# Kernel tuning notes

Hardware: AMD Instinct MI355X
Metric: run time of the kernel (lower is better)

The kernel has to match this reference:

```python
import jax, jax.numpy as jnp
import numpy as np

N_NODES = 100000
N_EDGES = 1600000
IN, HID, OUT = 128, 256, 64
EPS = 0.0  # init_eps=0, learn_eps=False


def setup_inputs() -> dict:
    key = jax.random.key(0)
    k1, k2, k3, k4, k5 = jax.random.split(key, 5)
    x = jax.random.normal(k1, (N_NODES, IN), dtype=jnp.float32)
    edge_src = jax.random.randint(k2, (N_EDGES,), 0, N_NODES, dtype=jnp.int64)
    edge_dst = jax.random.randint(k3, (N_EDGES,), 0, N_NODES, dtype=jnp.int64)
    W1 = jax.random.normal(k4, (IN, HID), dtype=jnp.float32) * (1.0 / np.sqrt(IN))
    W2 = jax.random.normal(k5, (HID, OUT), dtype=jnp.float32) * (1.0 / np.sqrt(HID))
    return {"x": x, "edge_src": edge_src, "edge_dst": edge_dst, "W1": W1, "W2": W2}


def _gin_conv(h, edge_src, edge_dst, W, n_nodes):
    # sum aggregation of messages h[src] into dst, then (1+eps)*h + agg, then linear (no bias)
    agg = jax.ops.segment_sum(h[edge_src], edge_dst, num_segments=n_nodes)
    return ((1.0 + EPS) * h + agg) @ W


def reference(x, edge_src, edge_dst, W1, W2):
    n = x.shape[0]
    h = _gin_conv(x, edge_src, edge_dst, W1, n)   # [N, HID]
    h = _gin_conv(h, edge_src, edge_dst, W2, n)   # [N, OUT]
    return h
```

## Files before the change

kernel.cpp:

```cpp
#include <hip/hip_runtime.h>
#include <hip/hip_bf16.h>

#define IN_F  128
#define HID_F 256
#define OUT_F 64
#define BUCKET_SHIFT 9
#define BUCKET_SZ 512
#define EPB 8192
#define CAP 10240

typedef __attribute__((ext_vector_type(8))) short bf16x8;
typedef __attribute__((ext_vector_type(4))) float f32x4;

__device__ __forceinline__ float bf2f(unsigned short u) {
    union { unsigned int i; float f; } v; v.i = ((unsigned int)u) << 16; return v.f;
}
__device__ __forceinline__ float bf2f_lo(unsigned int p) {
    union { unsigned int i; float f; } v; v.i = p << 16; return v.f;
}
__device__ __forceinline__ float bf2f_hi(unsigned int p) {
    union { unsigned int i; float f; } v; v.i = p & 0xffff0000u; return v.f;
}
__device__ __forceinline__ unsigned short f2bf(float f) {
    __hip_bfloat16 b = __float2bfloat16(f);
    return *reinterpret_cast<unsigned short*>(&b);
}

__global__ __launch_bounds__(256) void k_front(
    const float* __restrict__ x, unsigned short* __restrict__ xb, long long total8,
    const float* __restrict__ W1, const float* __restrict__ W2,
    unsigned short* __restrict__ w12s, int xBlocks)
{
    int bid = blockIdx.x;
    int t = threadIdx.x;
    if (bid < xBlocks) {
        long long i = (long long)bid * 256 + t;
        if (i >= total8) return;
        const float4* p = reinterpret_cast<const float4*>(x) + i * 2;
        float4 a = p[0], b = p[1];
        ushort4 o0, o1;
        o0.x = f2bf(a.x); o0.y = f2bf(a.y); o0.z = f2bf(a.z); o0.w = f2bf(a.w);
        o1.x = f2bf(b.x); o1.y = f2bf(b.y); o1.z = f2bf(b.z); o1.w = f2bf(b.w);
        reinterpret_cast<ushort4*>(xb)[i * 2]     = o0;
        reinterpret_cast<ushort4*>(xb)[i * 2 + 1] = o1;
    } else {
        int idx = (bid - xBlocks) * 256 + t;
        int c = idx >> 9, L = (idx >> 3) & 63, j = idx & 7;
        int nt = c >> 2, ks = c & 3;
        int k = ks * 32 + (L >> 4) * 8 + j;
        int n = nt * 16 + (L & 15);
        float s = 0.f;
        #pragma unroll 8
        for (int jj = 0; jj < HID_F; ++jj)
            s += W1[k * HID_F + jj] * W2[jj * OUT_F + n];
        w12s[idx] = f2bf(s);
    }
}

__global__ __launch_bounds__(256) void k_bin(
    const int* __restrict__ src, const int* __restrict__ dst,
    int* __restrict__ gcur, unsigned int* __restrict__ binned, int nEdges)
{
    __shared__ int hist[256];
    __shared__ int lcur[256];
    int t = threadIdx.x;
    hist[t] = 0;
    __syncthreads();
    long long base = (long long)blockIdx.x * EPB;
    #pragma unroll
    for (int k = 0; k < EPB / 256; ++k) {
        long long e = base + k * 256 + t;
        if (e < nEdges) atomicAdd(&hist[dst[e] >> BUCKET_SHIFT], 1);
    }
    __syncthreads();
    int h = hist[t];
    lcur[t] = (h > 0) ? atomicAdd(&gcur[t], h) : 0;
    __syncthreads();
    #pragma unroll
    for (int k = 0; k < EPB / 256; ++k) {
        long long e = base + k * 256 + t;
        if (e < nEdges) {
            int s = src[e], d = dst[e];
            int b = d >> BUCKET_SHIFT;
            int pos = atomicAdd(&lcur[b], 1);
            binned[(size_t)b * CAP + pos] =
                (((unsigned int)(d & (BUCKET_SZ - 1))) << 23) | (unsigned int)s;
        }
    }
}

__global__ __launch_bounds__(256) void k_localcsr(
    const unsigned int* __restrict__ binned, const int* __restrict__ gcur,
    int* __restrict__ rowbeg, int* __restrict__ rowend,
    int* __restrict__ eidx, int nNodes)
{
    __shared__ int ldeg[BUCKET_SZ];
    __shared__ int lscan[256];
    int t = threadIdx.x;
    ldeg[t] = 0; ldeg[t + 256] = 0;
    __syncthreads();
    int eb0 = blockIdx.x * CAP;
    int cnt = gcur[blockIdx.x];
    int node0 = blockIdx.x << BUCKET_SHIFT;
    for (int e = t; e < cnt; e += 256)
        atomicAdd(&ldeg[binned[eb0 + e] >> 23], 1);
    __syncthreads();
    int d0 = ldeg[2 * t], d1 = ldeg[2 * t + 1];
    int s = d0 + d1;
    lscan[t] = s;
    __syncthreads();
    for (int d = 1; d < 256; d <<= 1) {
        int add = (t >= d) ? lscan[t - d] : 0;
        __syncthreads();
        lscan[t] += add;
        __syncthreads();
    }
    int excl = lscan[t] - s;
    ldeg[2 * t]     = excl;
    ldeg[2 * t + 1] = excl + d0;
    int n0 = node0 + 2 * t;
    if (n0 < nNodes)     { rowbeg[n0]     = eb0 + excl;      rowend[n0]     = eb0 + excl + d0; }
    if (n0 + 1 < nNodes) { rowbeg[n0 + 1] = eb0 + excl + d0; rowend[n0 + 1] = eb0 + excl + d0 + d1; }
    __syncthreads();
    for (int e = t; e < cnt; e += 256) {
        unsigned int p = binned[eb0 + e];
        int dl = (int)(p >> 23), sv = (int)(p & 0x7fffffu);
        int pos = atomicAdd(&ldeg[dl], 1);
        eidx[eb0 + pos] = sv;
    }
}

__global__ __launch_bounds__(256) void gather1(
    const unsigned short* __restrict__ xb, const int* __restrict__ rowbeg,
    const int* __restrict__ rowend,
    const int* __restrict__ eidx, unsigned short* __restrict__ agg, int nNodes)
{
    int n    = blockIdx.x * 4 + __builtin_amdgcn_readfirstlane(threadIdx.x >> 6);
    int lane = threadIdx.x & 63;
    if (n >= nNodes) return;
    int beg = __builtin_amdgcn_readfirstlane(rowbeg[n]);
    int end = __builtin_amdgcn_readfirstlane(rowend[n]);
    int g = lane >> 4;
    int f = lane & 15;
    float acc[8] = {0.f, 0.f, 0.f, 0.f, 0.f, 0.f, 0.f, 0.f};

    for (int e0 = beg; e0 < end; e0 += 64) {
        int cnt = min(64, end - e0);
        int e = (lane < cnt) ? eidx[e0 + lane] : 0;
        for (int i = 0; i < cnt; i += 16) {
            uint4 v[4];
            unsigned int vmask[4];
            #pragma unroll
            for (int j = 0; j < 4; ++j) {
                int eij = i + 4 * j + g;
                int src = __builtin_amdgcn_ds_bpermute(eij << 2, e);
                int s0  = __builtin_amdgcn_readlane(e, i + 4 * j);
                bool valid = eij < cnt;
                vmask[j] = valid ? 0xffffffffu : 0u;
                src = valid ? src : s0;
                v[j] = *reinterpret_cast<const uint4*>(
                    xb + (unsigned)src * IN_F + (f << 3));
            }
            #pragma unroll
            for (int j = 0; j < 4; ++j) {
                unsigned int a0 = v[j].x & vmask[j], a1 = v[j].y & vmask[j];
                unsigned int a2 = v[j].z & vmask[j], a3 = v[j].w & vmask[j];
                acc[0] += bf2f_lo(a0); acc[1] += bf2f_hi(a0);
                acc[2] += bf2f_lo(a1); acc[3] += bf2f_hi(a1);
                acc[4] += bf2f_lo(a2); acc[5] += bf2f_hi(a2);
                acc[6] += bf2f_lo(a3); acc[7] += bf2f_hi(a3);
            }
        }
    }
    #pragma unroll
    for (int k = 0; k < 8; ++k) {
        acc[k] += __shfl_xor(acc[k], 16);
        acc[k] += __shfl_xor(acc[k], 32);
    }
    uint4 sv = *reinterpret_cast<const uint4*>(xb + (size_t)n * IN_F + (f << 3));
    acc[0] += bf2f_lo(sv.x); acc[1] += bf2f_hi(sv.x);
    acc[2] += bf2f_lo(sv.y); acc[3] += bf2f_hi(sv.y);
    acc[4] += bf2f_lo(sv.z); acc[5] += bf2f_hi(sv.z);
    acc[6] += bf2f_lo(sv.w); acc[7] += bf2f_hi(sv.w);
    if (g == 0) {
        uint4 o;
        o.x = (unsigned int)f2bf(acc[0]) | ((unsigned int)f2bf(acc[1]) << 16);
        o.y = (unsigned int)f2bf(acc[2]) | ((unsigned int)f2bf(acc[3]) << 16);
        o.z = (unsigned int)f2bf(acc[4]) | ((unsigned int)f2bf(acc[5]) << 16);
        o.w = (unsigned int)f2bf(acc[6]) | ((unsigned int)f2bf(acc[7]) << 16);
        *reinterpret_cast<uint4*>(agg + (size_t)n * IN_F + (f << 3)) = o;
    }
}

__global__ __launch_bounds__(256) void z_gemm(
    const unsigned short* __restrict__ agg,
    const unsigned short* __restrict__ w12s,
    unsigned short* __restrict__ z, int nNodes)
{
    int wave = threadIdx.x >> 6, lane = threadIdx.x & 63;
    int m0 = blockIdx.x * 64 + wave * 16;
    if (m0 >= nNodes) return;
    int row = lane & 15, quad = lane >> 4;
    f32x4 acc[4] = {};
    const bf16x8* aBase = reinterpret_cast<const bf16x8*>(
        agg + (size_t)(m0 + row) * IN_F + quad * 8);
    const bf16x8* bBase = reinterpret_cast<const bf16x8*>(w12s) + lane;
    #pragma unroll
    for (int ks = 0; ks < 4; ++ks) {
        bf16x8 a = aBase[ks * 4];
        #pragma unroll
        for (int nt = 0; nt < 4; ++nt) {
            bf16x8 b = bBase[(nt * 4 + ks) * 64];
            acc[nt] = __builtin_amdgcn_mfma_f32_16x16x32_bf16(a, b, acc[nt], 0, 0, 0);
        }
    }
    size_t outBase = (size_t)(m0 + quad * 4) * OUT_F + row;
    #pragma unroll
    for (int i = 0; i < 4; ++i) {
        if (m0 + quad * 4 + i >= nNodes) break;
        #pragma unroll
        for (int nt = 0; nt < 4; ++nt)
            z[outBase + (size_t)i * OUT_F + nt * 16] = f2bf(acc[nt][i]);
    }
}

__global__ __launch_bounds__(256) void gather2(
    const unsigned short* __restrict__ z, const int* __restrict__ rowbeg,
    const int* __restrict__ rowend,
    const int* __restrict__ eidx, float* __restrict__ out, int nNodes)
{
    int n    = blockIdx.x * 4 + __builtin_amdgcn_readfirstlane(threadIdx.x >> 6);
    int lane = threadIdx.x & 63;
    if (n >= nNodes) return;
    int beg = __builtin_amdgcn_readfirstlane(rowbeg[n]);
    int end = __builtin_amdgcn_readfirstlane(rowend[n]);
    int g = lane >> 3;
    int f = lane & 7;
    float acc[8] = {0.f, 0.f, 0.f, 0.f, 0.f, 0.f, 0.f, 0.f};

    for (int e0 = beg; e0 < end; e0 += 64) {
        int cnt = min(64, end - e0);
        int e = (lane < cnt) ? eidx[e0 + lane] : 0;
        for (int i = 0; i < cnt; i += 32) {
            uint4 v[4];
            unsigned int vmask[4];
            #pragma unroll
            for (int j = 0; j < 4; ++j) {
                int eij = i + 8 * j + g;
                int src = __builtin_amdgcn_ds_bpermute(eij << 2, e);
                int s0  = __builtin_amdgcn_readlane(e, i + 8 * j);
                bool valid = eij < cnt;
                vmask[j] = valid ? 0xffffffffu : 0u;
                src = valid ? src : s0;
                v[j] = *reinterpret_cast<const uint4*>(
                    z + (unsigned)src * OUT_F + (f << 3));
            }
            #pragma unroll
            for (int j = 0; j < 4; ++j) {
                unsigned int a0 = v[j].x & vmask[j], a1 = v[j].y & vmask[j];
                unsigned int a2 = v[j].z & vmask[j], a3 = v[j].w & vmask[j];
                acc[0] += bf2f_lo(a0); acc[1] += bf2f_hi(a0);
                acc[2] += bf2f_lo(a1); acc[3] += bf2f_hi(a1);
                acc[4] += bf2f_lo(a2); acc[5] += bf2f_hi(a2);
                acc[6] += bf2f_lo(a3); acc[7] += bf2f_hi(a3);
            }
        }
    }
    #pragma unroll
    for (int k = 0; k < 8; ++k) {
        acc[k] += __shfl_xor(acc[k], 8);
        acc[k] += __shfl_xor(acc[k], 16);
        acc[k] += __shfl_xor(acc[k], 32);
    }
    uint4 sv = *reinterpret_cast<const uint4*>(z + (size_t)n * OUT_F + (f << 3));
    acc[0] += bf2f_lo(sv.x); acc[1] += bf2f_hi(sv.x);
    acc[2] += bf2f_lo(sv.y); acc[3] += bf2f_hi(sv.y);
    acc[4] += bf2f_lo(sv.z); acc[5] += bf2f_hi(sv.z);
    acc[6] += bf2f_lo(sv.w); acc[7] += bf2f_hi(sv.w);
    if (g == 0) {
        float* o = out + (size_t)n * OUT_F + (f << 3);
        *reinterpret_cast<float4*>(o)     = make_float4(acc[0], acc[1], acc[2], acc[3]);
        *reinterpret_cast<float4*>(o + 4) = make_float4(acc[4], acc[5], acc[6], acc[7]);
    }
}

extern "C" void kernel_launch(void* const* d_in, const int* in_sizes, int n_in,
                              void* d_out, int out_size, void* d_ws, size_t ws_size,
                              hipStream_t stream) {
    const float* x  = (const float*)d_in[0];
    const int* esrc = (const int*)d_in[1];
    const int* edst = (const int*)d_in[2];
    const float* W1 = (const float*)d_in[3];
    const float* W2 = (const float*)d_in[4];
    float* out      = (float*)d_out;

    const int nNodes = in_sizes[0] / IN_F;
    const int nEdges = in_sizes[1];
    const int NB = (nNodes + BUCKET_SZ - 1) / BUCKET_SZ;
    const int A  = (nEdges + EPB - 1) / EPB;

    char* ws = (char*)d_ws;
    size_t off = 0;
    auto alloc = [&](size_t bytes) {
        char* p = ws + off; off = (off + bytes + 63) & ~(size_t)63; return p;
    };
    unsigned short* xb  = (unsigned short*)alloc((size_t)nNodes * IN_F * 2);
    unsigned short* agg = (unsigned short*)alloc((size_t)nNodes * IN_F * 2);
    unsigned short* z   = (unsigned short*)alloc((size_t)nNodes * OUT_F * 2);
    unsigned int* binned = (unsigned int*)alloc((size_t)NB * CAP * 4);
    int* eidx           = (int*)alloc((size_t)NB * CAP * 4);
    unsigned short* w12s = (unsigned short*)alloc((size_t)IN_F * OUT_F * 2);
    int* rowbeg         = (int*)alloc((size_t)nNodes * 4);
    int* rowend         = (int*)alloc((size_t)nNodes * 4);
    int* gcur           = (int*)alloc(256 * 4);

    hipMemsetAsync(gcur, 0, 256 * 4, stream);

    long long total8 = (long long)nNodes * IN_F / 8;
    const int xBlocks = (int)((total8 + 255) / 256);
    k_front<<<xBlocks + 32, 256, 0, stream>>>(
        x, xb, total8, W1, W2, w12s, xBlocks);

    k_bin<<<A, 256, 0, stream>>>(esrc, edst, gcur, binned, nEdges);
    k_localcsr<<<NB, 256, 0, stream>>>(binned, gcur, rowbeg, rowend, eidx, nNodes);

    const int nBlocks = (nNodes + 3) / 4;
    const int mBlocks = (nNodes + 63) / 64;
    gather1<<<nBlocks, 256, 0, stream>>>(xb, rowbeg, rowend, eidx, agg, nNodes);
    z_gemm<<<mBlocks, 256, 0, stream>>>(agg, w12s, z, nNodes);
    gather2<<<nBlocks, 256, 0, stream>>>(z, rowbeg, rowend, eidx, out, nNodes);
}
```

Baseline: 267.8 us.

## Fuse layer-1 gather with projection GEMM via LDS; widen binning/CSR blocks

Merges the first-layer neighbour gather and the 128x64 projection GEMM into one kernel. Each 1024-thread block gathers 16 node rows into a swizzled LDS tile, then four waves run MFMA on that tile. This removes the agg round trip through global memory and one launch. The binning and local CSR kernels also get larger blocks: 1024 threads with half the edges per block, and 512 threads with one node per thread. The risks are the extra block-wide sync in the fused kernel and lower occupancy from the large blocks.

```diff
diff --git a/kernel.cpp b/kernel.cpp
--- a/kernel.cpp
+++ b/kernel.cpp
@@ -6,7 +6,7 @@
 #define OUT_F 64
 #define BUCKET_SHIFT 9
 #define BUCKET_SZ 512
-#define EPB 8192
+#define EPB 4096
 #define CAP 10240
 
 typedef __attribute__((ext_vector_type(8))) short bf16x8;
@@ -57,28 +57,30 @@
     }
 }
 
-__global__ __launch_bounds__(256) void k_bin(
+__global__ __launch_bounds__(1024) void k_bin(
     const int* __restrict__ src, const int* __restrict__ dst,
     int* __restrict__ gcur, unsigned int* __restrict__ binned, int nEdges)
 {
     __shared__ int hist[256];
     __shared__ int lcur[256];
     int t = threadIdx.x;
-    hist[t] = 0;
+    if (t < 256) hist[t] = 0;
     __syncthreads();
     long long base = (long long)blockIdx.x * EPB;
     #pragma unroll
-    for (int k = 0; k < EPB / 256; ++k) {
-        long long e = base + k * 256 + t;
+    for (int k = 0; k < EPB / 1024; ++k) {
+        long long e = base + k * 1024 + t;
         if (e < nEdges) atomicAdd(&hist[dst[e] >> BUCKET_SHIFT], 1);
     }
     __syncthreads();
-    int h = hist[t];
-    lcur[t] = (h > 0) ? atomicAdd(&gcur[t], h) : 0;
+    if (t < 256) {
+        int h = hist[t];
+        lcur[t] = (h > 0) ? atomicAdd(&gcur[t], h) : 0;
+    }
     __syncthreads();
     #pragma unroll
-    for (int k = 0; k < EPB / 256; ++k) {
-        long long e = base + k * 256 + t;
+    for (int k = 0; k < EPB / 1024; ++k) {
+        long long e = base + k * 1024 + t;
         if (e < nEdges) {
             int s = src[e], d = dst[e];
             int b = d >> BUCKET_SHIFT;
@@ -89,40 +91,38 @@
     }
 }
 
-__global__ __launch_bounds__(256) void k_localcsr(
+__global__ __launch_bounds__(512) void k_localcsr(
     const unsigned int* __restrict__ binned, const int* __restrict__ gcur,
     int* __restrict__ rowbeg, int* __restrict__ rowend,
     int* __restrict__ eidx, int nNodes)
 {
     __shared__ int ldeg[BUCKET_SZ];
-    __shared__ int lscan[256];
+    __shared__ int lscan[BUCKET_SZ];
     int t = threadIdx.x;
-    ldeg[t] = 0; ldeg[t + 256] = 0;
+    ldeg[t] = 0;
     __syncthreads();
     int eb0 = blockIdx.x * CAP;
     int cnt = gcur[blockIdx.x];
     int node0 = blockIdx.x << BUCKET_SHIFT;
-    for (int e = t; e < cnt; e += 256)
+    for (int e = t; e < cnt; e += 512)
         atomicAdd(&ldeg[binned[eb0 + e] >> 23], 1);
     __syncthreads();
-    int d0 = ldeg[2 * t], d1 = ldeg[2 * t + 1];
-    int s = d0 + d1;
+    int s = ldeg[t];
     lscan[t] = s;
     __syncthreads();
-    for (int d = 1; d < 256; d <<= 1) {
+    for (int d = 1; d < 512; d <<= 1) {
         int add = (t >= d) ? lscan[t - d] : 0;
         __syncthreads();
         lscan[t] += add;
         __syncthreads();
     }
     int excl = lscan[t] - s;
-    ldeg[2 * t]     = excl;
-    ldeg[2 * t + 1] = excl + d0;
-    int n0 = node0 + 2 * t;
-    if (n0 < nNodes)     { rowbeg[n0]     = eb0 + excl;      rowend[n0]     = eb0 + excl + d0; }
-    if (n0 + 1 < nNodes) { rowbeg[n0 + 1] = eb0 + excl + d0; rowend[n0 + 1] = eb0 + excl + d0 + d1; }
-    __syncthreads();
-    for (int e = t; e < cnt; e += 256) {
+    int n0 = node0 + t;
+    if (n0 < nNodes) { rowbeg[n0] = eb0 + excl; rowend[n0] = eb0 + excl + s; }
+    __syncthreads();
+    ldeg[t] = excl;
+    __syncthreads();
+    for (int e = t; e < cnt; e += 512) {
         unsigned int p = binned[eb0 + e];
         int dl = (int)(p >> 23), sv = (int)(p & 0x7fffffu);
         int pos = atomicAdd(&ldeg[dl], 1);
@@ -130,97 +130,96 @@
     }
 }
 
-__global__ __launch_bounds__(256) void gather1(
+__global__ __launch_bounds__(1024) void gather1z(
     const unsigned short* __restrict__ xb, const int* __restrict__ rowbeg,
-    const int* __restrict__ rowend,
-    const int* __restrict__ eidx, unsigned short* __restrict__ agg, int nNodes)
-{
-    int n    = blockIdx.x * 4 + __builtin_amdgcn_readfirstlane(threadIdx.x >> 6);
-    int lane = threadIdx.x & 63;
-    if (n >= nNodes) return;
-    int beg = __builtin_amdgcn_readfirstlane(rowbeg[n]);
-    int end = __builtin_amdgcn_readfirstlane(rowend[n]);
+    const int* __restrict__ rowend, const int* __restrict__ eidx,
+    const unsigned short* __restrict__ w12s,
+    unsigned short* __restrict__ z, int nNodes)
+{
+    __shared__ unsigned short aggT[16 * IN_F];
+    int wave = threadIdx.x >> 6, lane = threadIdx.x & 63;
+    int m0 = blockIdx.x * 16;
+    int n = m0 + wave;
     int g = lane >> 4;
     int f = lane & 15;
-    float acc[8] = {0.f, 0.f, 0.f, 0.f, 0.f, 0.f, 0.f, 0.f};
-
-    for (int e0 = beg; e0 < end; e0 += 64) {
-        int cnt = min(64, end - e0);
-        int e = (lane < cnt) ? eidx[e0 + lane] : 0;
-        for (int i = 0; i < cnt; i += 16) {
-            uint4 v[4];
-            unsigned int vmask[4];
-            #pragma unroll
-            for (int j = 0; j < 4; ++j) {
-                int eij = i + 4 * j + g;
-                int src = __builtin_amdgcn_ds_bpermute(eij << 2, e);
-                int s0  = __builtin_amdgcn_readlane(e, i + 4 * j);
-                bool valid = eij < cnt;
-                vmask[j] = valid ? 0xffffffffu : 0u;
-                src = valid ? src : s0;
-                v[j] = *reinterpret_cast<const uint4*>(
-                    xb + (unsigned)src * IN_F + (f << 3));
+    char* sc = reinterpret_cast<char*>(aggT);
+
+    if (n < nNodes) {
+        int beg = __builtin_amdgcn_readfirstlane(rowbeg[n]);
+        int end = __builtin_amdgcn_readfirstlane(rowend[n]);
+        float acc[8] = {0.f, 0.f, 0.f, 0.f, 0.f, 0.f, 0.f, 0.f};
+        for (int e0 = beg; e0 < end; e0 += 64) {
+            int cnt = min(64, end - e0);
+            int e = (lane < cnt) ? eidx[e0 + lane] : 0;
+            for (int i = 0; i < cnt; i += 16) {
+                uint4 v[4];
+                unsigned int vmask[4];
+                #pragma unroll
+                for (int j = 0; j < 4; ++j) {
+                    int eij = i + 4 * j + g;
+                    int src = __builtin_amdgcn_ds_bpermute(eij << 2, e);
+                    int s0  = __builtin_amdgcn_readlane(e, i + 4 * j);
+                    bool valid = eij < cnt;
+                    vmask[j] = valid ? 0xffffffffu : 0u;
+                    src = valid ? src : s0;
+                    v[j] = *reinterpret_cast<const uint4*>(
+                        xb + (unsigned)src * IN_F + (f << 3));
+                }
+                #pragma unroll
+                for (int j = 0; j < 4; ++j) {
+                    unsigned int a0 = v[j].x & vmask[j], a1 = v[j].y & vmask[j];
+                    unsigned int a2 = v[j].z & vmask[j], a3 = v[j].w & vmask[j];
+                    acc[0] += bf2f_lo(a0); acc[1] += bf2f_hi(a0);
+                    acc[2] += bf2f_lo(a1); acc[3] += bf2f_hi(a1);
+                    acc[4] += bf2f_lo(a2); acc[5] += bf2f_hi(a2);
+                    acc[6] += bf2f_lo(a3); acc[7] += bf2f_hi(a3);
+                }
             }
-            #pragma unroll
-            for (int j = 0; j < 4; ++j) {
-                unsigned int a0 = v[j].x & vmask[j], a1 = v[j].y & vmask[j];
-                unsigned int a2 = v[j].z & vmask[j], a3 = v[j].w & vmask[j];
-                acc[0] += bf2f_lo(a0); acc[1] += bf2f_hi(a0);
-                acc[2] += bf2f_lo(a1); acc[3] += bf2f_hi(a1);
-                acc[4] += bf2f_lo(a2); acc[5] += bf2f_hi(a2);
-                acc[6] += bf2f_lo(a3); acc[7] += bf2f_hi(a3);
-            }
-        }
-    }
-    #pragma unroll
-    for (int k = 0; k < 8; ++k) {
-        acc[k] += __shfl_xor(acc[k], 16);
-        acc[k] += __shfl_xor(acc[k], 32);
-    }
-    uint4 sv = *reinterpret_cast<const uint4*>(xb + (size_t)n * IN_F + (f << 3));
-    acc[0] += bf2f_lo(sv.x); acc[1] += bf2f_hi(sv.x);
-    acc[2] += bf2f_lo(sv.y); acc[3] += bf2f_hi(sv.y);
-    acc[4] += bf2f_lo(sv.z); acc[5] += bf2f_hi(sv.z);
-    acc[6] += bf2f_lo(sv.w); acc[7] += bf2f_hi(sv.w);
-    if (g == 0) {
-        uint4 o;
-        o.x = (unsigned int)f2bf(acc[0]) | ((unsigned int)f2bf(acc[1]) << 16);
-        o.y = (unsigned int)f2bf(acc[2]) | ((unsigned int)f2bf(acc[3]) << 16);
-        o.z = (unsigned int)f2bf(acc[4]) | ((unsigned int)f2bf(acc[5]) << 16);
-        o.w = (unsigned int)f2bf(acc[6]) | ((unsigned int)f2bf(acc[7]) << 16);
-        *reinterpret_cast<uint4*>(agg + (size_t)n * IN_F + (f << 3)) = o;
-    }
-}
-
-__global__ __launch_bounds__(256) void z_gemm(
-    const unsigned short* __restrict__ agg,
-    const unsigned short* __restrict__ w12s,
-    unsigned short* __restrict__ z, int nNodes)
-{
-    int wave = threadIdx.x >> 6, lane = threadIdx.x & 63;
-    int m0 = blockIdx.x * 64 + wave * 16;
-    if (m0 >= nNodes) return;
-    int row = lane & 15, quad = lane >> 4;
-    f32x4 acc[4] = {};
-    const bf16x8* aBase = reinterpret_cast<const bf16x8*>(
-        agg + (size_t)(m0 + row) * IN_F + quad * 8);
-    const bf16x8* bBase = reinterpret_cast<const bf16x8*>(w12s) + lane;
-    #pragma unroll
-    for (int ks = 0; ks < 4; ++ks) {
-        bf16x8 a = aBase[ks * 4];
+        }
         #pragma unroll
-        for (int nt = 0; nt < 4; ++nt) {
-            bf16x8 b = bBase[(nt * 4 + ks) * 64];
-            acc[nt] = __builtin_amdgcn_mfma_f32_16x16x32_bf16(a, b, acc[nt], 0, 0, 0);
-        }
-    }
-    size_t outBase = (size_t)(m0 + quad * 4) * OUT_F + row;
-    #pragma unroll
-    for (int i = 0; i < 4; ++i) {
-        if (m0 + quad * 4 + i >= nNodes) break;
+        for (int k = 0; k < 8; ++k) {
+            acc[k] += __shfl_xor(acc[k], 16);
+            acc[k] += __shfl_xor(acc[k], 32);
+        }
+        uint4 sv = *reinterpret_cast<const uint4*>(xb + (size_t)n * IN_F + (f << 3));
+        acc[0] += bf2f_lo(sv.x); acc[1] += bf2f_hi(sv.x);
+        acc[2] += bf2f_lo(sv.y); acc[3] += bf2f_hi(sv.y);
+        acc[4] += bf2f_lo(sv.z); acc[5] += bf2f_hi(sv.z);
+        acc[6] += bf2f_lo(sv.w); acc[7] += bf2f_hi(sv.w);
+        if (g == 0) {
+            uint4 o;
+            o.x = (unsigned int)f2bf(acc[0]) | ((unsigned int)f2bf(acc[1]) << 16);
+            o.y = (unsigned int)f2bf(acc[2]) | ((unsigned int)f2bf(acc[3]) << 16);
+            o.z = (unsigned int)f2bf(acc[4]) | ((unsigned int)f2bf(acc[5]) << 16);
+            o.w = (unsigned int)f2bf(acc[6]) | ((unsigned int)f2bf(acc[7]) << 16);
+            int b = ((wave << 8) + (f << 4)) ^ ((wave & 7) << 4);
+            *reinterpret_cast<uint4*>(sc + b) = o;
+        }
+    } else {
+        if (g == 0) {
+            int b = ((wave << 8) + (f << 4)) ^ ((wave & 7) << 4);
+            *reinterpret_cast<uint4*>(sc + b) = make_uint4(0, 0, 0, 0);
+        }
+    }
+    __syncthreads();
+
+    if (wave < 4) {
+        int row = lane & 15, quad = lane >> 4;
+        f32x4 acc2 = {};
+        const bf16x8* bBase = reinterpret_cast<const bf16x8*>(w12s) + lane;
         #pragma unroll
-        for (int nt = 0; nt < 4; ++nt)
-            z[outBase + (size_t)i * OUT_F + nt * 16] = f2bf(acc[nt][i]);
+        for (int ks = 0; ks < 4; ++ks) {
+            int ab = ((row << 8) + (quad << 4) + (ks << 6)) ^ ((row & 7) << 4);
+            bf16x8 a = *reinterpret_cast<const bf16x8*>(sc + ab);
+            bf16x8 b = bBase[(wave * 4 + ks) * 64];
+            acc2 = __builtin_amdgcn_mfma_f32_16x16x32_bf16(a, b, acc2, 0, 0, 0);
+        }
+        size_t outBase = (size_t)(m0 + quad * 4) * OUT_F + wave * 16 + row;
+        #pragma unroll
+        for (int i = 0; i < 4; ++i) {
+            if (m0 + quad * 4 + i >= nNodes) break;
+            z[outBase + (size_t)i * OUT_F] = f2bf(acc2[i]);
+        }
     }
 }
 
@@ -305,7 +304,6 @@
         char* p = ws + off; off = (off + bytes + 63) & ~(size_t)63; return p;
     };
     unsigned short* xb  = (unsigned short*)alloc((size_t)nNodes * IN_F * 2);
-    unsigned short* agg = (unsigned short*)alloc((size_t)nNodes * IN_F * 2);
     unsigned short* z   = (unsigned short*)alloc((size_t)nNodes * OUT_F * 2);
     unsigned int* binned = (unsigned int*)alloc((size_t)NB * CAP * 4);
     int* eidx           = (int*)alloc((size_t)NB * CAP * 4);
@@ -321,12 +319,11 @@
     k_front<<<xBlocks + 32, 256, 0, stream>>>(
         x, xb, total8, W1, W2, w12s, xBlocks);
 
-    k_bin<<<A, 256, 0, stream>>>(esrc, edst, gcur, binned, nEdges);
-    k_localcsr<<<NB, 256, 0, stream>>>(binned, gcur, rowbeg, rowend, eidx, nNodes);
-
+    k_bin<<<A, 1024, 0, stream>>>(esrc, edst, gcur, binned, nEdges);
+    k_localcsr<<<NB, 512, 0, stream>>>(binned, gcur, rowbeg, rowend, eidx, nNodes);
+
+    const int g1Blocks = (nNodes + 15) / 16;
     const int nBlocks = (nNodes + 3) / 4;
-    const int mBlocks = (nNodes + 63) / 64;
-    gather1<<<nBlocks, 256, 0, stream>>>(xb, rowbeg, rowend, eidx, agg, nNodes);
-    z_gemm<<<mBlocks, 256, 0, stream>>>(agg, w12s, z, nNodes);
+    gather1z<<<g1Blocks, 1024, 0, stream>>>(xb, rowbeg, rowend, eidx, w12s, z, nNodes);
     gather2<<<nBlocks, 256, 0, stream>>>(z, rowbeg, rowend, eidx, out, nNodes);
 }
```

Result: faster. 255.9 us (-4.4%).
